# Kernel optimization log

Hardware: AMD Instinct MI355X
Metric: run time of the kernel (lower is better)

Reference implementation:

```python
import jax, jax.numpy as jnp
import numpy as np

N_VOICES = 8
N_PROFILES = 16
N_HARMONICS = 64
N_FRAMES = 64
N_SAMPLES = 2 ** 14  # 16384
SAMPLERATE = 22050
NYQUIST = SAMPLERATE / 2.0
MIN_FREQ = 40.0 / NYQUIST
# Reproduces the source's chained assignment `self.freq_interval = self.max_freq = self.min_freq`
FREQ_INTERVAL = MIN_FREQ
RATIOS = (np.arange(2, 2 + N_HARMONICS).astype(np.float32)) ** 2  # [64]


def _interp_linear(x, out_size):
    """torch F.interpolate(mode='linear', align_corners=False) along last axis."""
    n = x.shape[-1]
    scale = n / out_size
    coords = (jnp.arange(out_size, dtype=x.dtype) + 0.5) * scale - 0.5
    coords = jnp.clip(coords, 0.0, n - 1)
    lo = jnp.floor(coords).astype(jnp.int32)
    hi = jnp.minimum(lo + 1, n - 1)
    w = (coords - lo.astype(x.dtype))
    return x[..., lo] * (1.0 - w) + x[..., hi] * w


def setup_inputs() -> dict:
    key = jax.random.key(0)
    k1, k2, k3 = jax.random.split(key, 3)
    f0 = jax.random.normal(k1, (16, N_VOICES * 2, N_FRAMES), dtype=jnp.float32)
    harmonics = jax.random.normal(k2, (16, N_VOICES * N_PROFILES, N_FRAMES), dtype=jnp.float32)
    profiles = jax.random.uniform(k3, (N_PROFILES, N_HARMONICS), dtype=jnp.float32, minval=0.0, maxval=0.1)
    return {"f0": f0, "harmonics": harmonics, "profiles": profiles}


def reference(f0, harmonics, profiles):
    b = f0.shape[0]
    f0 = f0.reshape(b, N_VOICES, 2, N_FRAMES)
    harm = harmonics.reshape(b, N_VOICES, N_PROFILES, N_FRAMES)

    re, im = f0[:, :, 0, :], f0[:, :, 1, :]
    f0_amp = re * re + im * im                      # ||.||^2 over dim=-2, [b,v,f]
    ang = jnp.arctan2(im, re) / jnp.pi              # torch.angle(complex)/pi
    base = MIN_FREQ + (ang * ang) * FREQ_INTERVAL   # [b,v,f]

    ratios = jnp.asarray(RATIOS)
    hfreq = jnp.clip(base[:, :, None, :] * ratios[None, None, :, None], 0.0, 1.0)  # [b,v,h,f]

    w = jax.nn.softmax(harm, axis=2)                # softmax over profiles
    hamp = jnp.einsum('bvpf,ph->bvhf', w, profiles)
    hamp = jnp.clip(hamp, 0.0, 1.0) * f0_amp[:, :, None, :]

    full_freq = jnp.concatenate([base[:, :, None, :], hfreq], axis=2)
    full_amp = jnp.concatenate([f0_amp[:, :, None, :], hamp], axis=2)
    full_freq = full_freq.reshape(b * N_VOICES, N_HARMONICS + 1, N_FRAMES)
    full_amp = full_amp.reshape(b * N_VOICES, N_HARMONICS + 1, N_FRAMES)

    ff = _interp_linear(full_freq, N_SAMPLES)       # [b*v, 65, 16384]
    fa = _interp_linear(full_amp, N_SAMPLES)

    sig = fa * jnp.sin(jnp.cumsum(ff, axis=-1) * jnp.pi)
    sig = sig.reshape(b, N_VOICES, N_HARMONICS + 1, N_SAMPLES).sum(axis=(1, 2))
    return sig.reshape(b, 1, N_SAMPLES)
```

## Files before the change

kernel.cpp:

```cpp
#include <hip/hip_runtime.h>
#include <math.h>

#define NVOICE 8
#define NPROF  16
#define NHARM  64
#define NFRAME 64
#define NSAMP  16384
#define NB     16

#define NKEEP  16
#define NROWS2 (NVOICE * NKEEP)

__device__ __forceinline__ float min_freq() { return 40.0f / 11025.0f; }

__global__ __launch_bounds__(256)
void hm_fused(const float* __restrict__ f0,
              const float* __restrict__ harm,
              const float* __restrict__ prof,
              float* __restrict__ out)
{
    const int blk = blockIdx.x;
    const int b   = blk >> 5;
    const int cb  = blk & 31;
    const int c0  = cb * 2, c1 = c0 + 1;
    const int tid = threadIdx.x;

    __shared__ float  sBase[NVOICE][NFRAME + 1];
    __shared__ float  sAmp0[NVOICE][NFRAME + 1];
    __shared__ float  sProf[NPROF][NKEEP];
    __shared__ float  sW[NVOICE][4][NPROF];
    __shared__ float  sP[3][NROWS2];
    __shared__ float  sA[4][NROWS2];
    __shared__ float4 cf[2][2][NROWS2];
    __shared__ float  pf[2][2][NROWS2];

    if (tid < NPROF * NKEEP)
        sProf[tid >> 4][tid & 15] = prof[(tid >> 4) * NHARM + (tid & 15)];

    for (int idx = tid; idx < NVOICE * NFRAME; idx += 256) {
        const int v = idx >> 6, k = idx & 63;
        const float re  = f0[((size_t)b * 16 + 2 * v    ) * NFRAME + k];
        const float im  = f0[((size_t)b * 16 + 2 * v + 1) * NFRAME + k];
        const float ang = atan2f(im, re) * 0.3183098861837907f;
        sBase[v][k] = min_freq() + ang * ang * min_freq();
        sAmp0[v][k] = re * re + im * im;
    }
    __syncthreads();

    if (tid < NROWS2) {
        const int r = tid, v = r >> 4, h = r & 15;
        const float r2 = (float)((h + 1) * (h + 1));
        double p = 0.0;
        float prevF = 0.0f;
        for (int k = 0; k <= c1; ++k) {
            const float F = fminf(sBase[v][k] * r2, 1.0f);
            p += 64.0 * (double)(prevF + F);
            prevF = F;
            if (k == c0 - 1) sP[0][r] = (float)(p - floor(p));
            if (k == c0)     sP[1][r] = (float)(p - floor(p));
            if (k == c1)     sP[2][r] = (float)(p - floor(p));
        }
    } else if (tid < 128 + 32) {
        const int t2 = tid - 128;
        const int v = t2 >> 2, fi = t2 & 3;
        const int f = min(max(c0 - 1 + fi, 0), 63);
        float w[NPROF];
        float m = -INFINITY;
#pragma unroll
        for (int p = 0; p < NPROF; ++p) {
            w[p] = harm[((size_t)b * (NVOICE * NPROF) + v * NPROF + p) * NFRAME + f];
            m = fmaxf(m, w[p]);
        }
        float s = 0.0f;
#pragma unroll
        for (int p = 0; p < NPROF; ++p) { w[p] = expf(w[p] - m); s += w[p]; }
        const float inv = 1.0f / s;
#pragma unroll
        for (int p = 0; p < NPROF; ++p) sW[v][fi][p] = w[p] * inv;
    }
    __syncthreads();

    for (int idx = tid; idx < 4 * NROWS2; idx += 256) {
        const int fi = idx >> 7, r = idx & 127, v = r >> 4, h = r & 15;
        const int f = min(max(c0 - 1 + fi, 0), 63);
        const float a0 = sAmp0[v][f];
        float A = a0;
        if (h != 0) {
            float d = 0.0f;
#pragma unroll
            for (int p = 0; p < NPROF; ++p) d = fmaf(sW[v][fi][p], sProf[p][h - 1], d);
            A = fminf(fmaxf(d, 0.0f), 1.0f) * a0;
        }
        sA[fi][r] = A;
    }
    __syncthreads();

    for (int idx = tid; idx < 4 * NROWS2; idx += 256) {
        const int qh = idx >> 7, r = idx & 127;
        const int q = qh >> 1, hh = qh & 1;
        const int v = r >> 4, h = r & 15;
        const float r2 = (float)((h + 1) * (h + 1));
        const int fiA = q + hh, fiB = fiA + 1;
        const int fA = min(max(c0 - 1 + fiA, 0), 63);
        const int fB = min(max(c0 - 1 + fiB, 0), 63);
        const float Fa = 0.5f * fminf(sBase[v][fA] * r2, 1.0f);
        const float Fb = 0.5f * fminf(sBase[v][fB] * r2, 1.0f);
        const float Aa = sA[fiA][r], Ab = sA[fiB][r];
        cf[q][hh][r] = make_float4(Fa, Fb - Fa, Aa, Ab - Aa);
        pf[q][hh][r] = (hh == 0) ? ((c0 + q == 0) ? 0.0f : sP[q][r])
                                 : sP[q + 1][r];
    }
    __syncthreads();

    const int q = tid >> 7;
    const int h = (tid >> 6) & 1;
    const int l = tid & 63;
    const int c = c0 + q;

    const int j0 = l + (h ? 0 : 128);
    const int j1 = j0 + 64;

    float t1a = (float)(j0 + 1);
    float t1b = (float)(j1 + 1);
    const float t2a = (float)((j0 + 1) * (j0 + 1)) * (1.0f / 512.0f);
    const float t2b = (float)((j1 + 1) * (j1 + 1)) * (1.0f / 512.0f);
    const float t3a = ((float)j0 + 0.5f) * (1.0f / 256.0f);
    const float t3b = ((float)j1 + 0.5f) * (1.0f / 256.0f);
    if (c == 0 && h == 0) {
        t1a = (float)(l + 1);
        t1b = (float)(l + 65);
    }

    const float4* __restrict__ V = cf[q][h];
    const float*  __restrict__ P = pf[q][h];

    float acc0 = 0.0f, acc1 = 0.0f;
#pragma unroll 4
    for (int r = 0; r < NROWS2; ++r) {
        const float4 vv = V[r];
        const float  pp = P[r];
        const float x0 = fmaf(t2a, vv.y, fmaf(t1a, vv.x, pp));
        const float x1 = fmaf(t2b, vv.y, fmaf(t1b, vv.x, pp));
        const float fa0 = fmaf(t3a, vv.w, vv.z);
        const float fa1 = fmaf(t3b, vv.w, vv.z);
        acc0 = fmaf(fa0, __builtin_amdgcn_sinf(__builtin_amdgcn_fractf(x0)), acc0);
        acc1 = fmaf(fa1, __builtin_amdgcn_sinf(__builtin_amdgcn_fractf(x1)), acc1);
    }

    float* o = out + (size_t)b * NSAMP + c * 256 + h * 128 + l;
    o[0]  = acc0;
    o[64] = acc1;
}

extern "C" void kernel_launch(void* const* d_in, const int* in_sizes, int n_in,
                              void* d_out, int out_size, void* d_ws, size_t ws_size,
                              hipStream_t stream)
{
    const float* f0   = (const float*)d_in[0];
    const float* harm = (const float*)d_in[1];
    const float* prof = (const float*)d_in[2];

    hm_fused<<<NB * 32, 256, 0, stream>>>(f0, harm, prof, (float*)d_out);
}
```

Measured before the change: 18.01 us.

## Split fused kernel into per-chunk coefficient builder and wide synthesis kernel

The single fused kernel is split in two. A setup kernel computes per-chunk interpolation coefficients and phase offsets for 8 chunks per block and writes them to workspace. A separate synthesis kernel then runs 2048 small 64-thread blocks that read those records from global memory. This amortizes the redundant per-block setup (atan2, softmax, serial phase prefix) over more chunks, at the cost of a second launch, a global-memory round trip and a longer serial phase loop per setup block.

```diff
diff --git a/kernel.cpp b/kernel.cpp
--- a/kernel.cpp
+++ b/kernel.cpp
@@ -14,28 +14,27 @@
 __device__ __forceinline__ float min_freq() { return 40.0f / 11025.0f; }
 
 __global__ __launch_bounds__(256)
-void hm_fused(const float* __restrict__ f0,
-              const float* __restrict__ harm,
-              const float* __restrict__ prof,
-              float* __restrict__ out)
+void hm_recs(const float* __restrict__ f0,
+             const float* __restrict__ harm,
+             const float* __restrict__ prof,
+             float4* __restrict__ rec4,
+             float* __restrict__ recP)
 {
-    const int blk = blockIdx.x;
-    const int b   = blk >> 5;
-    const int cb  = blk & 31;
-    const int c0  = cb * 2, c1 = c0 + 1;
-    const int tid = threadIdx.x;
+    const int blk  = blockIdx.x;
+    const int b    = blk >> 3;
+    const int o    = blk & 7;
+    const int c_lo = 8 * o;
+    const int c_hi = c_lo + 7;
+    const int tid  = threadIdx.x;
 
-    __shared__ float  sBase[NVOICE][NFRAME + 1];
-    __shared__ float  sAmp0[NVOICE][NFRAME + 1];
-    __shared__ float  sProf[NPROF][NKEEP];
-    __shared__ float  sW[NVOICE][4][NPROF];
-    __shared__ float  sP[3][NROWS2];
-    __shared__ float  sA[4][NROWS2];
-    __shared__ float4 cf[2][2][NROWS2];
-    __shared__ float  pf[2][2][NROWS2];
+    __shared__ float sBase[NVOICE][NFRAME];
+    __shared__ float sAmp0[NVOICE][NFRAME];
+    __shared__ float sProf[NPROF][NKEEP];
+    __shared__ float sW[NVOICE][10][NPROF];
+    __shared__ float sPP[9][NROWS2];
+    __shared__ float sA[10][NROWS2];
 
-    if (tid < NPROF * NKEEP)
-        sProf[tid >> 4][tid & 15] = prof[(tid >> 4) * NHARM + (tid & 15)];
+    sProf[tid >> 4][tid & 15] = prof[(tid >> 4) * NHARM + (tid & 15)];
 
     for (int idx = tid; idx < NVOICE * NFRAME; idx += 256) {
         const int v = idx >> 6, k = idx & 63;
@@ -45,25 +44,25 @@
         sBase[v][k] = min_freq() + ang * ang * min_freq();
         sAmp0[v][k] = re * re + im * im;
     }
+    if (c_lo == 0 && tid < NROWS2) sPP[0][tid] = 0.0f;
     __syncthreads();
 
     if (tid < NROWS2) {
-        const int r = tid, v = r >> 4, h = r & 15;
-        const float r2 = (float)((h + 1) * (h + 1));
+        const int r = tid, v = r >> 4, hh = r & 15;
+        const float r2 = (float)((hh + 1) * (hh + 1));
         double p = 0.0;
         float prevF = 0.0f;
-        for (int k = 0; k <= c1; ++k) {
+        for (int k = 0; k <= c_hi; ++k) {
             const float F = fminf(sBase[v][k] * r2, 1.0f);
             p += 64.0 * (double)(prevF + F);
             prevF = F;
-            if (k == c0 - 1) sP[0][r] = (float)(p - floor(p));
-            if (k == c0)     sP[1][r] = (float)(p - floor(p));
-            if (k == c1)     sP[2][r] = (float)(p - floor(p));
+            const int fi = k - (c_lo - 1);
+            if (fi >= 0) sPP[fi][r] = (float)(p - floor(p));
         }
-    } else if (tid < 128 + 32) {
-        const int t2 = tid - 128;
-        const int v = t2 >> 2, fi = t2 & 3;
-        const int f = min(max(c0 - 1 + fi, 0), 63);
+    } else if (tid < 128 + 80) {
+        const int t = tid - 128;
+        const int v = t / 10, fi = t % 10;
+        const int f = min(max(c_lo - 1 + fi, 0), 63);
         float w[NPROF];
         float m = -INFINITY;
 #pragma unroll
@@ -80,62 +79,73 @@
     }
     __syncthreads();
 
-    for (int idx = tid; idx < 4 * NROWS2; idx += 256) {
-        const int fi = idx >> 7, r = idx & 127, v = r >> 4, h = r & 15;
-        const int f = min(max(c0 - 1 + fi, 0), 63);
+    for (int idx = tid; idx < 10 * NROWS2; idx += 256) {
+        const int fi = idx >> 7, r = idx & 127, v = r >> 4, hh = r & 15;
+        const int f = min(max(c_lo - 1 + fi, 0), 63);
         const float a0 = sAmp0[v][f];
         float A = a0;
-        if (h != 0) {
+        if (hh != 0) {
             float d = 0.0f;
 #pragma unroll
-            for (int p = 0; p < NPROF; ++p) d = fmaf(sW[v][fi][p], sProf[p][h - 1], d);
+            for (int p = 0; p < NPROF; ++p) d = fmaf(sW[v][fi][p], sProf[p][hh - 1], d);
             A = fminf(fmaxf(d, 0.0f), 1.0f) * a0;
         }
         sA[fi][r] = A;
     }
     __syncthreads();
 
-    for (int idx = tid; idx < 4 * NROWS2; idx += 256) {
-        const int qh = idx >> 7, r = idx & 127;
-        const int q = qh >> 1, hh = qh & 1;
-        const int v = r >> 4, h = r & 15;
-        const float r2 = (float)((h + 1) * (h + 1));
-        const int fiA = q + hh, fiB = fiA + 1;
-        const int fA = min(max(c0 - 1 + fiA, 0), 63);
-        const int fB = min(max(c0 - 1 + fiB, 0), 63);
+    for (int idx = tid; idx < 16 * NROWS2; idx += 256) {
+        const int crel = idx >> 8;
+        const int rest = idx & 255;
+        const int hh   = rest >> 7;
+        const int r    = rest & 127;
+        const int v    = r >> 4, hr = r & 15;
+        const float r2 = (float)((hr + 1) * (hr + 1));
+        const int c  = c_lo + crel;
+        const int fA = min(max(c - 1 + hh, 0), 63);
+        const int fB = min(c + hh, 63);
         const float Fa = 0.5f * fminf(sBase[v][fA] * r2, 1.0f);
         const float Fb = 0.5f * fminf(sBase[v][fB] * r2, 1.0f);
+        const int fiA = crel + hh, fiB = fiA + 1;
         const float Aa = sA[fiA][r], Ab = sA[fiB][r];
-        cf[q][hh][r] = make_float4(Fa, Fb - Fa, Aa, Ab - Aa);
-        pf[q][hh][r] = (hh == 0) ? ((c0 + q == 0) ? 0.0f : sP[q][r])
-                                 : sP[q + 1][r];
+        const size_t oidx = ((((size_t)b * 64 + c) * 2 + hh) * NROWS2) + r;
+        rec4[oidx] = make_float4(Fa, Fb - Fa, Aa, Ab - Aa);
+        recP[oidx] = (c == 0 && hh == 0) ? 0.0f : sPP[crel + hh][r];
     }
-    __syncthreads();
+}
 
-    const int q = tid >> 7;
-    const int h = (tid >> 6) & 1;
-    const int l = tid & 63;
-    const int c = c0 + q;
+__global__ __launch_bounds__(64)
+void hm_synth(const float4* __restrict__ rec4,
+              const float* __restrict__ recP,
+              float* __restrict__ out)
+{
+    const int blk  = blockIdx.x;
+    const int b    = blk >> 7;
+    const int rest = blk & 127;
+    const int c    = rest >> 1;
+    const int h    = rest & 1;
+    const int l    = threadIdx.x;
 
     const int j0 = l + (h ? 0 : 128);
     const int j1 = j0 + 64;
 
     float t1a = (float)(j0 + 1);
     float t1b = (float)(j1 + 1);
+    if (c == 0 && h == 0) {
+        t1a = (float)(l + 1);
+        t1b = (float)(l + 65);
+    }
     const float t2a = (float)((j0 + 1) * (j0 + 1)) * (1.0f / 512.0f);
     const float t2b = (float)((j1 + 1) * (j1 + 1)) * (1.0f / 512.0f);
     const float t3a = ((float)j0 + 0.5f) * (1.0f / 256.0f);
     const float t3b = ((float)j1 + 0.5f) * (1.0f / 256.0f);
-    if (c == 0 && h == 0) {
-        t1a = (float)(l + 1);
-        t1b = (float)(l + 65);
-    }
 
-    const float4* __restrict__ V = cf[q][h];
-    const float*  __restrict__ P = pf[q][h];
+    const size_t base = (((size_t)b * 64 + c) * 2 + h) * NROWS2;
+    const float4* __restrict__ V = rec4 + base;
+    const float*  __restrict__ P = recP + base;
 
     float acc0 = 0.0f, acc1 = 0.0f;
-#pragma unroll 4
+#pragma unroll 8
     for (int r = 0; r < NROWS2; ++r) {
         const float4 vv = V[r];
         const float  pp = P[r];
@@ -160,5 +170,9 @@
     const float* harm = (const float*)d_in[1];
     const float* prof = (const float*)d_in[2];
 
-    hm_fused<<<NB * 32, 256, 0, stream>>>(f0, harm, prof, (float*)d_out);
+    float4* rec4 = (float4*)d_ws;
+    float*  recP = (float*)((char*)d_ws + (size_t)NB * 64 * 2 * NROWS2 * sizeof(float4));
+
+    hm_recs<<<NB * 8, 256, 0, stream>>>(f0, harm, prof, rec4, recP);
+    hm_synth<<<NB * 128, 64, 0, stream>>>(rec4, recP, (float*)d_out);
 }
```

Measured after the change: 23.68 us. 31.5% more time.
